# Kernel tuning notes

Measured on AMD Instinct MI355X. Metric: run time of the kernel, lower is better.

## Reference

```python
import jax, jax.numpy as jnp
import numpy as np

B, T, C, H, E, TOPK, DR = 2, 2048, 768, 3072, 8, 2, 24


def setup_inputs() -> dict:
    key = jax.random.key(0)
    ks = jax.random.split(key, 16)
    std = 0.02
    n = lambda k, shape, s=std: (s * jax.random.normal(k, shape)).astype(jnp.float32)
    emb = jax.random.normal(ks[3], (E, DR), dtype=jnp.float32)
    emb = emb / (jnp.linalg.norm(emb, axis=-1, keepdims=True) + 1e-8)
    return {
        "x": jax.random.normal(ks[0], (B, T, C), dtype=jnp.float32),
        "router_w": n(ks[1], (E, C)),
        "probe_w": n(ks[2], (DR, C)),
        "router_emb": emb,
        "fatigue": jnp.zeros((E,), jnp.float32),
        "energy": jnp.ones((E,), jnp.float32),
        "w_fast1": n(ks[4], (E, C, H)),
        "w_slow1": n(ks[5], (E, C, H)),
        "h_fast1": n(ks[6], (E, C, H), 0.005),
        "m_gate1": jax.random.uniform(ks[7], (E,), dtype=jnp.float32),
        "b1": jnp.zeros((E, H), jnp.float32),
        "w_fast2": n(ks[8], (E, H, C)),
        "w_slow2": n(ks[9], (E, H, C)),
        "h_fast2": n(ks[10], (E, H, C), 0.005),
        "m_gate2": jax.random.uniform(ks[11], (E,), dtype=jnp.float32),
        "b2": jnp.zeros((E, C), jnp.float32),
    }


def _normalize(v, axis=-1, eps=1e-12):
    # matches F.normalize: v / max(||v||, eps)
    return v / jnp.maximum(jnp.linalg.norm(v, axis=axis, keepdims=True), eps)


def reference(x, router_w, probe_w, router_emb, fatigue, energy,
              w_fast1, w_slow1, h_fast1, m_gate1, b1,
              w_fast2, w_slow2, h_fast2, m_gate2, b2):
    Bd, Td, Cd = x.shape
    # --- router logits with biology-inspired biases ---
    logits = jnp.einsum('btc,ec->bte', x, router_w)            # nn.Linear, no bias
    tok_proxy = x.mean(axis=-1, keepdims=True)                  # [B,T,1]
    router_gain = jnp.linalg.norm(router_emb, axis=-1)          # [E]
    base_bias = 0.02 * tok_proxy                                # broadcasts over E
    gain_bias = 0.02 * tok_proxy * router_gain                  # [B,T,E]
    tok_unit = _normalize(jnp.einsum('btc,dc->btd', x, probe_w))
    align_bias = 0.02 * jnp.einsum('btd,ed->bte', tok_unit, _normalize(router_emb))
    logits = logits + base_bias + gain_bias + align_bias + 0.1 * energy - 0.1 * fatigue
    # --- top-k gating ---
    g, idx = jax.lax.top_k(logits, TOPK)                        # [B,T,K]
    gates = jax.nn.softmax(g, axis=-1)
    N = Bd * Td
    gates_full = jnp.zeros((N, E), x.dtype).at[
        jnp.arange(N)[:, None], idx.reshape(N, TOPK)].set(gates.reshape(N, TOPK))
    flat_x = x.reshape(N, Cd)
    # --- expert dispatch: dynamic W = w_fast + m_gate*w_slow + H_fast ---
    def body(acc, p):
        wf1, ws1, hf1, mg1, bb1, wf2, ws2, hf2, mg2, bb2, ge = p
        W1 = wf1 + mg1 * ws1 + hf1                              # [C,H]
        h = jnp.square(jnp.maximum(flat_x @ W1 + bb1, 0.0))     # relu(y)^2
        W2 = wf2 + mg2 * ws2 + hf2                              # [H,C]
        y = h @ W2 + bb2
        return acc + ge[:, None] * y, None
    out, _ = jax.lax.scan(
        body, jnp.zeros((N, Cd), x.dtype),
        (w_fast1, w_slow1, h_fast1, m_gate1, b1,
         w_fast2, w_slow2, h_fast2, m_gate2, b2, gates_full.T))
    return out.reshape(Bd, Td, Cd)
```

## Files before the change

kernel.cpp:

```cpp
#include <hip/hip_runtime.h>

typedef unsigned short u16;
typedef __attribute__((ext_vector_type(8))) short short8;
typedef __attribute__((ext_vector_type(8))) unsigned short ushort8;
typedef __attribute__((ext_vector_type(4))) unsigned short ushort4v;
typedef __attribute__((ext_vector_type(4))) float f32x4;

static constexpr int Cdim = 768;
static constexpr int Hdim = 3072;
static constexpr int Edim = 8;
static constexpr int Ntok = 4096;
static constexpr int DRc  = 24;
static constexpr int NSLOT = Ntok * 2;
static constexpr int NCHUNK = 8;
static constexpr int CCH = Cdim / NCHUNK;
static constexpr int KS2 = 3;
static constexpr int KC2 = Hdim / KS2;

static constexpr size_t OFF_XB   = 0;
static constexpr size_t OFF_W1T  = 6291456;
static constexpr size_t OFF_W2T  = 44040192;
static constexpr size_t OFF_HBUF = 81788928;
static constexpr size_t OFF_XT   = OFF_HBUF;
static constexpr size_t OFF_PART = OFF_HBUF + 12582912;
static constexpr size_t OFF_YB   = OFF_W1T;
static constexpr size_t OFF_TOK  = 132120576;
static constexpr size_t OFF_CNT  = 132382720;
static constexpr size_t OFF_OFFS = 132382752;
static constexpr size_t OFF_TSLOT= 132382784;
static constexpr size_t OFF_TG   = 132448320;

__device__ __forceinline__ u16 f2bf(float f) {
  unsigned u = __builtin_bit_cast(unsigned, f);
  u += 0x7fffu + ((u >> 16) & 1u);
  return (u16)(u >> 16);
}

__device__ __forceinline__ float bf2f(u16 v) {
  unsigned u = ((unsigned)v) << 16;
  return __builtin_bit_cast(float, u);
}

__device__ __forceinline__ void gld16(const u16* g, u16* l) {
  __builtin_amdgcn_global_load_lds((const __attribute__((address_space(1))) unsigned int*)g,
                                   (__attribute__((address_space(3))) unsigned int*)l,
                                   16, 0, 0);
}

__global__ __launch_bounds__(256)
void prep_x2_kernel(const float* __restrict__ x, u16* __restrict__ x16,
                    float* __restrict__ xT) {
  __shared__ float tile[64][65];
  const int c0 = blockIdx.x * 64;
  const int t0 = blockIdx.y * 64;
  const int tid = threadIdx.x;
  const int row = tid >> 4, col = (tid & 15) * 4;
  #pragma unroll
  for (int i = 0; i < 4; i++) {
    int r = row + i * 16;
    size_t idx = (size_t)(t0 + r) * Cdim + c0 + col;
    float4 v = *(const float4*)(x + idx);
    tile[r][col + 0] = v.x; tile[r][col + 1] = v.y;
    tile[r][col + 2] = v.z; tile[r][col + 3] = v.w;
    ushort4v o = { f2bf(v.x), f2bf(v.y), f2bf(v.z), f2bf(v.w) };
    *reinterpret_cast<ushort4v*>(x16 + idx) = o;
  }
  __syncthreads();
  const int c = tid >> 2, tg = (tid & 3) * 16;
  #pragma unroll
  for (int q = 0; q < 4; q++) {
    float4 w;
    w.x = tile[tg + q * 4 + 0][c];
    w.y = tile[tg + q * 4 + 1][c];
    w.z = tile[tg + q * 4 + 2][c];
    w.w = tile[tg + q * 4 + 3][c];
    *reinterpret_cast<float4*>(xT + (size_t)(c0 + c) * Ntok + t0 + tg + q * 4) = w;
  }
}

__global__ __launch_bounds__(256)
void prep_wt_kernel(const float* __restrict__ wf, const float* __restrict__ wsl,
                    const float* __restrict__ hf, const float* __restrict__ mg,
                    u16* __restrict__ outw, const int R, const int Ccol) {
  __shared__ u16 tileT[64][66];
  const int e = blockIdx.z;
  const int r0 = blockIdx.x * 64, c0 = blockIdx.y * 64;
  const float m = mg[e];
  const size_t base = (size_t)e * R * Ccol;
  const int t = threadIdx.x;
  const int cr = t >> 4, cc = (t & 15) * 4;
  #pragma unroll
  for (int i = 0; i < 4; i++) {
    int r = cr + i * 16;
    size_t idx = base + (size_t)(r0 + r) * Ccol + (c0 + cc);
    float4 a = *(const float4*)(wf + idx);
    float4 b = *(const float4*)(wsl + idx);
    float4 h = *(const float4*)(hf + idx);
    tileT[cc + 0][r] = f2bf(fmaf(m, b.x, a.x) + h.x);
    tileT[cc + 1][r] = f2bf(fmaf(m, b.y, a.y) + h.y);
    tileT[cc + 2][r] = f2bf(fmaf(m, b.z, a.z) + h.z);
    tileT[cc + 3][r] = f2bf(fmaf(m, b.w, a.w) + h.w);
  }
  __syncthreads();
  const int oc = t >> 2, ch = (t & 3) * 16;
  ushort8 o0, o1;
  #pragma unroll
  for (int j = 0; j < 8; j++) { o0[j] = tileT[oc][ch + j]; o1[j] = tileT[oc][ch + 8 + j]; }
  size_t oidx = ((size_t)e * Ccol + c0 + oc) * R + r0 + ch;
  *reinterpret_cast<ushort8*>(outw + oidx) = o0;
  *reinterpret_cast<ushort8*>(outw + oidx + 8) = o1;
}

__global__ __launch_bounds__(256)
void logits_part_kernel(const float* __restrict__ xT, const float* __restrict__ router_w,
                        const float* __restrict__ probe_w, float* __restrict__ part) {
  const int t = blockIdx.x * 256 + threadIdx.x;
  const int cB = blockIdx.y * CCH;
  float racc[Edim] = {};
  float pacc[DRc] = {};
  float sacc = 0.f;
  for (int ci = 0; ci < CCH; ci++) {
    int c = cB + ci;
    float xv = xT[(size_t)c * Ntok + t];
    sacc += xv;
    #pragma unroll
    for (int ee = 0; ee < Edim; ee++) racc[ee] = fmaf(xv, router_w[ee * Cdim + c], racc[ee]);
    #pragma unroll
    for (int d = 0; d < DRc; d++) pacc[d] = fmaf(xv, probe_w[d * Cdim + c], pacc[d]);
  }
  float* pb = part + (size_t)blockIdx.y * 33 * Ntok + t;
  #pragma unroll
  for (int ee = 0; ee < Edim; ee++) pb[(size_t)ee * Ntok] = racc[ee];
  #pragma unroll
  for (int d = 0; d < DRc; d++) pb[(size_t)(8 + d) * Ntok] = pacc[d];
  pb[(size_t)32 * Ntok] = sacc;
}

__global__ __launch_bounds__(256)
void router_fin_kernel(const float* __restrict__ part, const float* __restrict__ emb,
                       const float* __restrict__ fatigue, const float* __restrict__ energy,
                       int* __restrict__ counts, int* __restrict__ tok_list,
                       int4* __restrict__ tokslot, float2* __restrict__ tokgate) {
  const int t = blockIdx.x * 256 + threadIdx.x;
  float v[33];
  #pragma unroll
  for (int o = 0; o < 33; o++) {
    float s = 0.f;
    #pragma unroll
    for (int ch = 0; ch < NCHUNK; ch++)
      s += part[((size_t)ch * 33 + o) * Ntok + t];
    v[o] = s;
  }
  const float* racc = v;
  const float* pacc = v + 8;
  float proxy = v[32] / 768.f;
  float pn2 = 0.f;
  #pragma unroll
  for (int d = 0; d < DRc; d++) pn2 += pacc[d] * pacc[d];
  float pnorm = sqrtf(pn2);
  float logitv[Edim];
  #pragma unroll
  for (int ee = 0; ee < Edim; ee++) {
    float g2 = 0.f, dote = 0.f;
    #pragma unroll
    for (int d = 0; d < DRc; d++) {
      float ev = emb[ee * DRc + d];
      g2 += ev * ev;
      dote += pacc[d] * ev;
    }
    float gain = sqrtf(g2);
    float align = dote / (fmaxf(pnorm, 1e-12f) * fmaxf(gain, 1e-12f));
    logitv[ee] = racc[ee] + 0.02f * proxy * (1.f + gain) + 0.02f * align
               + 0.1f * energy[ee] - 0.1f * fatigue[ee];
  }
  int e0 = 0; float b0v = logitv[0];
  #pragma unroll
  for (int ee = 1; ee < Edim; ee++) if (logitv[ee] > b0v) { b0v = logitv[ee]; e0 = ee; }
  int e1 = -1; float b1v = -3.4e38f;
  #pragma unroll
  for (int ee = 0; ee < Edim; ee++) if (ee != e0 && logitv[ee] > b1v) { b1v = logitv[ee]; e1 = ee; }
  float texp = expf(b1v - b0v);
  float g0 = 1.f / (1.f + texp);
  float g1 = texp / (1.f + texp);
  int p0 = atomicAdd(&counts[e0], 1);
  tok_list[e0 * Ntok + p0] = t;
  int p1 = atomicAdd(&counts[e1], 1);
  tok_list[e1 * Ntok + p1] = t;
  tokslot[t] = make_int4(e0, p0, e1, p1);
  tokgate[t] = make_float2(g0, g1);
}

__global__ void offsets_kernel(const int* __restrict__ counts, int* __restrict__ offs) {
  if (threadIdx.x == 0) {
    int r = 0;
    for (int e = 0; e < Edim; e++) { offs[e] = r; r += counts[e]; }
  }
}

__global__ __launch_bounds__(256)
void fc1_kernel(const u16* __restrict__ x16, const u16* __restrict__ W1T,
                const float* __restrict__ b1, const int* __restrict__ counts,
                const int* __restrict__ offs, const int* __restrict__ tok_list,
                u16* __restrict__ h_buf) {
  const int e = blockIdx.z;
  const int n_e = counts[e];
  const int tokBase = blockIdx.y * 128;
  if (tokBase >= n_e) return;
  const int hBase = blockIdx.x * 128;
  __shared__ u16 As[2][4096];
  __shared__ u16 Bs[2][4096];
  __shared__ int toks[128];
  const int tid = threadIdx.x;
  if (tid < 128) {
    int s = tokBase + tid;
    toks[tid] = (s < n_e) ? tok_list[e * Ntok + s] : 0;
  }
  __syncthreads();
  const int lane = tid & 63, wv = tid >> 6;
  const int wr = wv >> 1, wc = wv & 1;
  const int sRow = lane >> 2, sSlot = lane & 3;
  const int kbOff = (sSlot ^ ((sRow >> 1) & 3)) * 8;
  const int rA0 = wv * 16 + sRow, rA1 = 64 + rA0;
  const u16* pA0 = x16 + (size_t)toks[rA0] * Cdim + kbOff;
  const u16* pA1 = x16 + (size_t)toks[rA1] * Cdim + kbOff;
  const u16* pB0 = W1T + ((size_t)e * Hdim + hBase + rA0) * Cdim + kbOff;
  const u16* pB1 = W1T + ((size_t)e * Hdim + hBase + rA1) * Cdim + kbOff;
  const int stOff = wv * 512 + lane * 8;
  const int fr = lane & 15;
  const int qsw = (((lane >> 4) ^ ((fr >> 1) & 3))) * 8;
  f32x4 acc[4][4] = {};
  gld16(pA0, &As[0][stOff]);
  gld16(pA1, &As[0][2048 + stOff]);
  gld16(pB0, &Bs[0][stOff]);
  gld16(pB1, &Bs[0][2048 + stOff]);
  __syncthreads();
  int cur = 0;
  for (int it = 0; it < 24; it++) {
    if (it < 23) {
      int k1 = (it + 1) * 32;
      gld16(pA0 + k1, &As[cur ^ 1][stOff]);
      gld16(pA1 + k1, &As[cur ^ 1][2048 + stOff]);
      gld16(pB0 + k1, &Bs[cur ^ 1][stOff]);
      gld16(pB1 + k1, &Bs[cur ^ 1][2048 + stOff]);
    }
    short8 aF[4], bF[4];
    #pragma unroll
    for (int m = 0; m < 4; m++)
      aF[m] = *reinterpret_cast<const short8*>(&As[cur][(wr * 64 + m * 16 + fr) * 32 + qsw]);
    #pragma unroll
    for (int n = 0; n < 4; n++)
      bF[n] = *reinterpret_cast<const short8*>(&Bs[cur][(wc * 64 + n * 16 + fr) * 32 + qsw]);
    #pragma unroll
    for (int m = 0; m < 4; m++)
      #pragma unroll
      for (int n = 0; n < 4; n++)
        acc[m][n] = __builtin_amdgcn_mfma_f32_16x16x32_bf16(aF[m], bF[n], acc[m][n], 0, 0, 0);
    __syncthreads();
    cur ^= 1;
  }
  const int rq = (lane >> 4) * 4;
  float bias[4];
  #pragma unroll
  for (int n = 0; n < 4; n++) bias[n] = b1[(size_t)e * Hdim + hBase + wc * 64 + n * 16 + fr];
  const int rowB = offs[e] + tokBase;
  #pragma unroll
  for (int m = 0; m < 4; m++) {
    #pragma unroll
    for (int j = 0; j < 4; j++) {
      int rl = wr * 64 + m * 16 + rq + j;
      if (tokBase + rl < n_e) {
        size_t rb = (size_t)(rowB + rl) * Hdim + hBase + wc * 64 + fr;
        #pragma unroll
        for (int n = 0; n < 4; n++) {
          float v = fmaxf(acc[m][n][j] + bias[n], 0.f);
          h_buf[rb + n * 16] = f2bf(v * v);
        }
      }
    }
  }
}

__global__ __launch_bounds__(256)
void fc2_kernel(const u16* __restrict__ h_buf, const u16* __restrict__ W2T,
                const float* __restrict__ b2, const int* __restrict__ counts,
                const int* __restrict__ offs, u16* __restrict__ ybuf) {
  const int e = blockIdx.z;
  const int n_e = counts[e];
  const int tokBase = blockIdx.y * 128;
  if (tokBase >= n_e) return;
  const int xb = blockIdx.x;
  const int kch = xb / 6;
  const int cBase = (xb % 6) * 128;
  const size_t kOff = (size_t)kch * KC2;
  __shared__ u16 As[2][4096];
  __shared__ u16 Bs[2][4096];
  const int tid = threadIdx.x;
  const int lane = tid & 63, wv = tid >> 6;
  const int wr = wv >> 1, wc = wv & 1;
  const int sRow = lane >> 2, sSlot = lane & 3;
  const int kbOff = (sSlot ^ ((sRow >> 1) & 3)) * 8;
  const int rA0 = wv * 16 + sRow, rA1 = 64 + rA0;
  const int slotB = offs[e] + tokBase;
  const int s0 = min(slotB + rA0, NSLOT - 1);
  const int s1 = min(slotB + rA1, NSLOT - 1);
  const u16* pA0 = h_buf + (size_t)s0 * Hdim + kOff + kbOff;
  const u16* pA1 = h_buf + (size_t)s1 * Hdim + kOff + kbOff;
  const u16* pB0 = W2T + ((size_t)e * Cdim + cBase + rA0) * Hdim + kOff + kbOff;
  const u16* pB1 = W2T + ((size_t)e * Cdim + cBase + rA1) * Hdim + kOff + kbOff;
  const int stOff = wv * 512 + lane * 8;
  const int fr = lane & 15;
  const int qsw = (((lane >> 4) ^ ((fr >> 1) & 3))) * 8;
  f32x4 acc[4][4] = {};
  gld16(pA0, &As[0][stOff]);
  gld16(pA1, &As[0][2048 + stOff]);
  gld16(pB0, &Bs[0][stOff]);
  gld16(pB1, &Bs[0][2048 + stOff]);
  __syncthreads();
  int cur = 0;
  for (int it = 0; it < KC2 / 32; it++) {
    if (it < KC2 / 32 - 1) {
      int k1 = (it + 1) * 32;
      gld16(pA0 + k1, &As[cur ^ 1][stOff]);
      gld16(pA1 + k1, &As[cur ^ 1][2048 + stOff]);
      gld16(pB0 + k1, &Bs[cur ^ 1][stOff]);
      gld16(pB1 + k1, &Bs[cur ^ 1][2048 + stOff]);
    }
    short8 aF[4], bF[4];
    #pragma unroll
    for (int m = 0; m < 4; m++)
      aF[m] = *reinterpret_cast<const short8*>(&As[cur][(wr * 64 + m * 16 + fr) * 32 + qsw]);
    #pragma unroll
    for (int n = 0; n < 4; n++)
      bF[n] = *reinterpret_cast<const short8*>(&Bs[cur][(wc * 64 + n * 16 + fr) * 32 + qsw]);
    #pragma unroll
    for (int m = 0; m < 4; m++)
      #pragma unroll
      for (int n = 0; n < 4; n++)
        acc[m][n] = __builtin_amdgcn_mfma_f32_16x16x32_bf16(aF[m], bF[n], acc[m][n], 0, 0, 0);
    __syncthreads();
    cur ^= 1;
  }
  const int rq = (lane >> 4) * 4;
  float bias[4];
  #pragma unroll
  for (int n = 0; n < 4; n++)
    bias[n] = (kch == 0) ? b2[(size_t)e * Cdim + cBase + wc * 64 + n * 16 + fr] : 0.f;
  u16* yb = ybuf + (size_t)kch * NSLOT * Cdim;
  #pragma unroll
  for (int m = 0; m < 4; m++) {
    #pragma unroll
    for (int j = 0; j < 4; j++) {
      int rl = wr * 64 + m * 16 + rq + j;
      if (tokBase + rl < n_e) {
        u16* ob = yb + (size_t)(slotB + rl) * Cdim + cBase + wc * 64 + fr;
        #pragma unroll
        for (int n = 0; n < 4; n++)
          ob[n * 16] = f2bf(acc[m][n][j] + bias[n]);
      }
    }
  }
}

__global__ __launch_bounds__(256)
void gather_kernel(const u16* __restrict__ ybuf, const int4* __restrict__ tokslot,
                   const float2* __restrict__ tokgate, const int* __restrict__ offs,
                   float* __restrict__ out) {
  const int gid = blockIdx.x * 256 + threadIdx.x;
  const int t = gid / 192;
  const int c4 = (gid - t * 192) * 4;
  int4 ts = tokslot[t];
  float2 g = tokgate[t];
  size_t s0 = (size_t)(offs[ts.x] + ts.y) * Cdim + c4;
  size_t s1 = (size_t)(offs[ts.z] + ts.w) * Cdim + c4;
  const size_t K1 = (size_t)NSLOT * Cdim;
  float acc0[4] = {}, acc1[4] = {};
  #pragma unroll
  for (int k = 0; k < KS2; k++) {
    ushort4v a = *reinterpret_cast<const ushort4v*>(ybuf + k * K1 + s0);
    ushort4v b = *reinterpret_cast<const ushort4v*>(ybuf + k * K1 + s1);
    #pragma unroll
    for (int j = 0; j < 4; j++) { acc0[j] += bf2f(a[j]); acc1[j] += bf2f(b[j]); }
  }
  float4 o;
  o.x = g.x * acc0[0] + g.y * acc1[0];
  o.y = g.x * acc0[1] + g.y * acc1[1];
  o.z = g.x * acc0[2] + g.y * acc1[2];
  o.w = g.x * acc0[3] + g.y * acc1[3];
  *reinterpret_cast<float4*>(out + (size_t)t * Cdim + c4) = o;
}

extern "C" void kernel_launch(void* const* d_in, const int* in_sizes, int n_in,
                              void* d_out, int out_size, void* d_ws, size_t ws_size,
                              hipStream_t stream) {
  const float* x        = (const float*)d_in[0];
  const float* router_w = (const float*)d_in[1];
  const float* probe_w  = (const float*)d_in[2];
  const float* emb      = (const float*)d_in[3];
  const float* fatigue  = (const float*)d_in[4];
  const float* energy   = (const float*)d_in[5];
  const float* wf1      = (const float*)d_in[6];
  const float* ws1      = (const float*)d_in[7];
  const float* hf1      = (const float*)d_in[8];
  const float* mg1      = (const float*)d_in[9];
  const float* b1       = (const float*)d_in[10];
  const float* wf2      = (const float*)d_in[11];
  const float* ws2      = (const float*)d_in[12];
  const float* hf2      = (const float*)d_in[13];
  const float* mg2      = (const float*)d_in[14];
  const float* b2       = (const float*)d_in[15];
  float* out = (float*)d_out;
  char* ws = (char*)d_ws;

  u16*    x16       = (u16*)(ws + OFF_XB);
  u16*    W1T       = (u16*)(ws + OFF_W1T);
  u16*    W2T       = (u16*)(ws + OFF_W2T);
  u16*    hbuf      = (u16*)(ws + OFF_HBUF);
  float*  xT        = (float*)(ws + OFF_XT);
  float*  part      = (float*)(ws + OFF_PART);
  u16*    ybuf      = (u16*)(ws + OFF_YB);
  int*    tok_list  = (int*)(ws + OFF_TOK);
  int*    counts    = (int*)(ws + OFF_CNT);
  int*    offs      = (int*)(ws + OFF_OFFS);
  int4*   tokslot   = (int4*)(ws + OFF_TSLOT);
  float2* tokgate   = (float2*)(ws + OFF_TG);

  hipMemsetAsync(counts, 0, 64, stream);

  prep_x2_kernel<<<dim3(Cdim / 64, Ntok / 64), 256, 0, stream>>>(x, x16, xT);
  logits_part_kernel<<<dim3(Ntok / 256, NCHUNK), 256, 0, stream>>>(xT, router_w, probe_w, part);
  router_fin_kernel<<<Ntok / 256, 256, 0, stream>>>(part, emb, fatigue, energy,
                                                    counts, tok_list, tokslot, tokgate);
  prep_wt_kernel<<<dim3(Cdim / 64, Hdim / 64, Edim), 256, 0, stream>>>(wf1, ws1, hf1, mg1, W1T, Cdim, Hdim);
  prep_wt_kernel<<<dim3(Hdim / 64, Cdim / 64, Edim), 256, 0, stream>>>(wf2, ws2, hf2, mg2, W2T, Hdim, Cdim);
  offsets_kernel<<<1, 64, 0, stream>>>(counts, offs);
  fc1_kernel<<<dim3(Hdim / 128, Ntok / 128, Edim), 256, 0, stream>>>(x16, W1T, b1, counts, offs,
                                                                     tok_list, hbuf);
  fc2_kernel<<<dim3(6 * KS2, Ntok / 128, Edim), 256, 0, stream>>>(hbuf, W2T, b2, counts, offs,
                                                                  ybuf);
  gather_kernel<<<Ntok * 192 / 256, 256, 0, stream>>>(ybuf, tokslot, tokgate, offs, out);
  (void)in_sizes; (void)n_in; (void)out_size; (void)ws_size;
}
```

Before: 366.7 us.

## Compact expert GEMM grids via row map and XCD-aware block remapping

Builds a compact list of (expert, token-tile) rows in the offsets kernel, so the fc1 and fc2 grids are 1D over at most 71 real rows instead of a padded 3D grid. Most blocks in the old grid exit early because they are empty. Block ids are also remapped so that consecutive logical tiles land on the same XCD, aiming to improve L2 reuse of weight and activation tiles. A fixed MAXROWS bound of 71 is assumed; if the routed rows exceed it, the result is wrong. A few blocks may still launch and exit when rows are fewer.

```diff
diff --git a/kernel.cpp b/kernel.cpp
--- a/kernel.cpp
+++ b/kernel.cpp
@@ -16,6 +16,7 @@
 static constexpr int CCH = Cdim / NCHUNK;
 static constexpr int KS2 = 3;
 static constexpr int KC2 = Hdim / KS2;
+static constexpr int MAXROWS = 71;
 
 static constexpr size_t OFF_XB   = 0;
 static constexpr size_t OFF_W1T  = 6291456;
@@ -25,6 +26,8 @@
 static constexpr size_t OFF_PART = OFF_HBUF + 12582912;
 static constexpr size_t OFF_YB   = OFF_W1T;
 static constexpr size_t OFF_TOK  = 132120576;
+static constexpr size_t OFF_RM   = 132251648;
+static constexpr size_t OFF_NR   = 132252160;
 static constexpr size_t OFF_CNT  = 132382720;
 static constexpr size_t OFF_OFFS = 132382752;
 static constexpr size_t OFF_TSLOT= 132382784;
@@ -45,6 +48,12 @@
   __builtin_amdgcn_global_load_lds((const __attribute__((address_space(1))) unsigned int*)g,
                                    (__attribute__((address_space(3))) unsigned int*)l,
                                    16, 0, 0);
+}
+
+__device__ __forceinline__ int xcd_remap(int p, int nwg) {
+  int q = nwg >> 3, rem = nwg & 7;
+  int x = p & 7, i = p >> 3;
+  return (x < rem ? x * (q + 1) : rem * (q + 1) + (x - rem) * q) + i;
 }
 
 __global__ __launch_bounds__(256)
@@ -190,10 +199,17 @@
   tokgate[t] = make_float2(g0, g1);
 }
 
-__global__ void offsets_kernel(const int* __restrict__ counts, int* __restrict__ offs) {
+__global__ void offsets_kernel(const int* __restrict__ counts, int* __restrict__ offs,
+                               int* __restrict__ rowmap, int* __restrict__ nrows) {
   if (threadIdx.x == 0) {
-    int r = 0;
-    for (int e = 0; e < Edim; e++) { offs[e] = r; r += counts[e]; }
+    int r = 0, nr = 0;
+    for (int e = 0; e < Edim; e++) {
+      offs[e] = r;
+      int ne = counts[e];
+      for (int tb = 0; tb < ne; tb += 128) rowmap[nr++] = (e << 16) | (tb >> 7);
+      r += ne;
+    }
+    nrows[0] = nr;
   }
 }
 
@@ -201,12 +217,17 @@
 void fc1_kernel(const u16* __restrict__ x16, const u16* __restrict__ W1T,
                 const float* __restrict__ b1, const int* __restrict__ counts,
                 const int* __restrict__ offs, const int* __restrict__ tok_list,
+                const int* __restrict__ rowmap, const int* __restrict__ nrows,
                 u16* __restrict__ h_buf) {
-  const int e = blockIdx.z;
+  const int l = xcd_remap(blockIdx.x, MAXROWS * 24);
+  const int r = l / 24;
+  if (r >= nrows[0]) return;
+  const int hB = l % 24;
+  const int rm = rowmap[r];
+  const int e = rm >> 16;
+  const int tokBase = (rm & 0xffff) << 7;
   const int n_e = counts[e];
-  const int tokBase = blockIdx.y * 128;
-  if (tokBase >= n_e) return;
-  const int hBase = blockIdx.x * 128;
+  const int hBase = hB * 128;
   __shared__ u16 As[2][4096];
   __shared__ u16 Bs[2][4096];
   __shared__ int toks[128];
@@ -283,12 +304,16 @@
 __global__ __launch_bounds__(256)
 void fc2_kernel(const u16* __restrict__ h_buf, const u16* __restrict__ W2T,
                 const float* __restrict__ b2, const int* __restrict__ counts,
-                const int* __restrict__ offs, u16* __restrict__ ybuf) {
-  const int e = blockIdx.z;
+                const int* __restrict__ offs, const int* __restrict__ rowmap,
+                const int* __restrict__ nrows, u16* __restrict__ ybuf) {
+  const int l = xcd_remap(blockIdx.x, MAXROWS * 18);
+  const int r = l / 18;
+  if (r >= nrows[0]) return;
+  const int xb = l % 18;
+  const int rm = rowmap[r];
+  const int e = rm >> 16;
+  const int tokBase = (rm & 0xffff) << 7;
   const int n_e = counts[e];
-  const int tokBase = blockIdx.y * 128;
-  if (tokBase >= n_e) return;
-  const int xb = blockIdx.x;
   const int kch = xb / 6;
   const int cBase = (xb % 6) * 128;
   const size_t kOff = (size_t)kch * KC2;
@@ -419,6 +444,8 @@
   float*  part      = (float*)(ws + OFF_PART);
   u16*    ybuf      = (u16*)(ws + OFF_YB);
   int*    tok_list  = (int*)(ws + OFF_TOK);
+  int*    rowmap    = (int*)(ws + OFF_RM);
+  int*    nrows     = (int*)(ws + OFF_NR);
   int*    counts    = (int*)(ws + OFF_CNT);
   int*    offs      = (int*)(ws + OFF_OFFS);
   int4*   tokslot   = (int4*)(ws + OFF_TSLOT);
@@ -432,11 +459,11 @@
                                                     counts, tok_list, tokslot, tokgate);
   prep_wt_kernel<<<dim3(Cdim / 64, Hdim / 64, Edim), 256, 0, stream>>>(wf1, ws1, hf1, mg1, W1T, Cdim, Hdim);
   prep_wt_kernel<<<dim3(Hdim / 64, Cdim / 64, Edim), 256, 0, stream>>>(wf2, ws2, hf2, mg2, W2T, Hdim, Cdim);
-  offsets_kernel<<<1, 64, 0, stream>>>(counts, offs);
-  fc1_kernel<<<dim3(Hdim / 128, Ntok / 128, Edim), 256, 0, stream>>>(x16, W1T, b1, counts, offs,
-                                                                     tok_list, hbuf);
-  fc2_kernel<<<dim3(6 * KS2, Ntok / 128, Edim), 256, 0, stream>>>(hbuf, W2T, b2, counts, offs,
-                                                                  ybuf);
+  offsets_kernel<<<1, 64, 0, stream>>>(counts, offs, rowmap, nrows);
+  fc1_kernel<<<MAXROWS * 24, 256, 0, stream>>>(x16, W1T, b1, counts, offs, tok_list,
+                                               rowmap, nrows, hbuf);
+  fc2_kernel<<<MAXROWS * 18, 256, 0, stream>>>(hbuf, W2T, b2, counts, offs,
+                                               rowmap, nrows, ybuf);
   gather_kernel<<<Ntok * 192 / 256, 256, 0, stream>>>(ybuf, tokslot, tokgate, offs, out);
   (void)in_sizes; (void)n_in; (void)out_size; (void)ws_size;
 }
```

Result: faster. 353.3 us (-3.7%).
